# Performance work log

Hardware: AMD Instinct MI355X
Metric: run time of the kernel (lower is better)

The kernel has to match this reference:

```python
import jax, jax.numpy as jnp
import numpy as np
from jax import lax


def conv2d(x, w, b=None, pad=1):
    y = lax.conv_general_dilated(x, w, (1, 1), [(pad, pad), (pad, pad)],
                                 dimension_numbers=('NCHW', 'OIHW', 'NCHW'))
    return y if b is None else y + b[None, :, None, None]


def conv3d(x, w, b=None, pad=(0, 0, 0), dil=(1, 1, 1), groups=1):
    y = lax.conv_general_dilated(x, w, (1, 1, 1), [(p, p) for p in pad],
                                 rhs_dilation=dil,
                                 dimension_numbers=('NCDHW', 'OIDHW', 'NCDHW'),
                                 feature_group_count=groups)
    return y if b is None else y + b[None, :, None, None, None]


def base_grid(H, W, dtype):
    # normalized grid, channel 0 = x in [-1,1], channel 1 = y in [-1,1]
    gxn = 2.0 * jnp.arange(W, dtype=dtype) / max(W - 1, 1) - 1.0
    gyn = 2.0 * jnp.arange(H, dtype=dtype) / max(H - 1, 1) - 1.0
    return jnp.stack([jnp.broadcast_to(gxn[None, :], (H, W)),
                      jnp.broadcast_to(gyn[:, None], (H, W))], 0)


def grid_sample(img, grid):
    # img (N,C,H,W), grid (N,H,W,2) in [-1,1] (x,y); bilinear, zeros padding, align_corners=False
    N, C, H, W = img.shape
    gx = ((grid[..., 0] + 1.0) * W - 1.0) * 0.5
    gy = ((grid[..., 1] + 1.0) * H - 1.0) * 0.5
    x0 = jnp.floor(gx)
    y0 = jnp.floor(gy)
    wx = gx - x0
    wy = gy - y0

    def one(im, x0b, y0b, wxb, wyb):
        x0i = x0b.astype(jnp.int32)
        y0i = y0b.astype(jnp.int32)

        def samp(xi, yi):
            valid = (xi >= 0) & (xi < W) & (yi >= 0) & (yi < H)
            v = im[:, jnp.clip(yi, 0, H - 1), jnp.clip(xi, 0, W - 1)]
            return v * valid[None].astype(im.dtype)

        v00 = samp(x0i, y0i)
        v01 = samp(x0i + 1, y0i)
        v10 = samp(x0i, y0i + 1)
        v11 = samp(x0i + 1, y0i + 1)
        return (v00 * (1 - wxb) * (1 - wyb) + v01 * wxb * (1 - wyb)
                + v10 * (1 - wxb) * wyb + v11 * wxb * wyb)

    return jax.vmap(one)(img, x0, y0, wx, wy)


def ms_def_corr(x, y, off):
    # deformable correlation: per scale, warp y by that scale's offset and take
    # the channel-mean dot product with x -> (BT, S, H, W)
    BT, C, H, W = x.shape
    base = base_grid(H, W, x.dtype)
    sc = jnp.array([W - 1, H - 1], x.dtype)[None, :, None, None]
    S = off.shape[1] // 2
    corrs = []
    for i in range(S):
        vg = base[None] + off[:, 2 * i:2 * i + 2] / sc
        w = grid_sample(y, vg.transpose(0, 2, 3, 1))
        corrs.append(jnp.mean(x * w, axis=1))
    return jnp.stack(corrs, 1)


def corr_filter(corr, w1, w2):
    avg = jnp.mean(corr, 1, keepdims=True)
    mx = jnp.max(corr, 1, keepdims=True)
    var = jnp.var(corr, axis=1, keepdims=True, ddof=1)  # torch.var unbiased
    attn = jax.nn.sigmoid(conv2d(jnp.concatenate([avg, mx], 1), w1) + conv2d(var, w2))
    return corr * attn


def setup_inputs() -> dict:
    key = jax.random.key(0)
    ks = jax.random.split(key, 16)
    B, C, T, H, W = 2, 64, 16, 64, 64
    S = 3
    r = C // 16

    def n(k, shape, s=0.02):
        return jax.random.normal(k, shape, jnp.float32) * s

    return {
        'x': jax.random.normal(ks[0], (B, C, T, H, W), jnp.float32),
        'ofs_l_w1': n(ks[1], (C, 2 * C, 3, 3)), 'ofs_l_b1': jnp.zeros((C,), jnp.float32),
        'ofs_l_w2': n(ks[2], (2 * S, C, 3, 3)), 'ofs_l_b2': jnp.zeros((2 * S,), jnp.float32),
        'ofs_r_w1': n(ks[3], (C, 2 * C, 3, 3)), 'ofs_r_b1': jnp.zeros((C,), jnp.float32),
        'ofs_r_w2': n(ks[4], (2 * S, C, 3, 3)), 'ofs_r_b2': jnp.zeros((2 * S,), jnp.float32),
        'cf_w1': n(ks[5], (1, 2, 3, 3), 0.1), 'cf_w2': n(ks[6], (1, 1, 3, 3), 0.1),
        'down_w': n(ks[7], (r, C, 1, 1, 1), 0.1),
        'sa1_w': n(ks[8], (r, 1, 9, 3, 3), 0.1), 'sa1_b': jnp.zeros((r,), jnp.float32),
        'sa2_w': n(ks[9], (r, 1, 9, 3, 3), 0.1), 'sa2_b': jnp.zeros((r,), jnp.float32),
        'sa3_w': n(ks[10], (r, 1, 9, 3, 3), 0.1), 'sa3_b': jnp.zeros((r,), jnp.float32),
        'agg_w': jnp.ones((3,), jnp.float32) / 3,
        'back_w': n(ks[11], (C, r, 1, 1, 1), 0.1),
        'fusion_w': jnp.ones((2,), jnp.float32) / 2,
    }


def reference(x, ofs_l_w1, ofs_l_b1, ofs_l_w2, ofs_l_b2,
              ofs_r_w1, ofs_r_b1, ofs_r_w2, ofs_r_b2,
              cf_w1, cf_w2, down_w,
              sa1_w, sa1_b, sa2_w, sa2_b, sa3_w, sa3_b,
              agg_w, back_w, fusion_w):
    B, C, T, H, W = x.shape
    r = down_w.shape[0]

    # long-term branch: 1x1x1 down conv -> 3 dilated depthwise 3D convs -> 1x1x1 up conv
    x_agg = conv3d(x, down_w)
    agg = (conv3d(x_agg, sa1_w, sa1_b, (4, 1, 1), (1, 1, 1), r) * agg_w[0]
           + conv3d(x_agg, sa2_w, sa2_b, (4, 2, 2), (1, 2, 2), r) * agg_w[1]
           + conv3d(x_agg, sa3_w, sa3_b, (4, 3, 3), (1, 3, 3), r) * agg_w[2])
    long_term = jax.nn.sigmoid(conv3d(agg, back_w)) - 0.5

    # temporal shifts
    left = jnp.concatenate([x[:, :, 1:], x[:, :, -1:]], 2)
    right = jnp.concatenate([x[:, :, :1], x[:, :, :-1]], 2)
    xf = x.transpose(0, 2, 1, 3, 4).reshape(B * T, C, H, W)
    lf = left.transpose(0, 2, 1, 3, 4).reshape(B * T, C, H, W)
    rf = right.transpose(0, 2, 1, 3, 4).reshape(B * T, C, H, W)

    off_lm = conv2d(jax.nn.relu(conv2d(jnp.concatenate([xf, lf], 1), ofs_l_w1, ofs_l_b1)),
                    ofs_l_w2, ofs_l_b2)
    off_rm = conv2d(jax.nn.relu(conv2d(jnp.concatenate([xf, rf], 1), ofs_r_w1, ofs_r_b1)),
                    ofs_r_w2, ofs_r_b2)

    corr_lm = ms_def_corr(xf, lf, off_lm)
    corr_rm = ms_def_corr(xf, rf, off_rm)
    fcl = corr_filter(corr_lm, cf_w1, cf_w2)
    fcr = corr_filter(corr_rm, cf_w1, cf_w2)

    base = base_grid(H, W, x.dtype)
    sc = jnp.array([W - 1, H - 1], x.dtype)[None, :, None, None]
    vg_lm = base[None] + off_lm[:, :2] / sc
    vg_rm = base[None] + off_rm[:, :2] / sc
    warped_lm = grid_sample(lf, vg_lm.transpose(0, 2, 3, 1))
    warped_rm = grid_sample(rf, vg_rm.transpose(0, 2, 3, 1))

    attn_lm = jnp.mean(fcl, 1, keepdims=True)
    attn_rm = jnp.mean(fcr, 1, keepdims=True)
    feat_lm = warped_lm * (jax.nn.sigmoid(attn_lm) - 0.5)
    feat_rm = warped_rm * (jax.nn.sigmoid(attn_rm) - 0.5)

    short = fusion_w[0] * feat_lm + fusion_w[1] * feat_rm
    short = short.reshape(B, T, C, H, W).transpose(0, 2, 1, 3, 4)
    return short * long_term
```

## Files before the change

kernel.cpp:

```cpp
#include <hip/hip_runtime.h>
#include <hip/hip_bf16.h>
#include <math.h>


typedef __attribute__((ext_vector_type(8))) short short8v;
typedef __attribute__((ext_vector_type(4))) float f32x4;

__device__ __forceinline__ float sigmoidf_(float v) {
    return 1.0f / (1.0f + expf(-v));
}

__device__ __forceinline__ float bf2f(short s) {
    union { unsigned u; float f; } z;
    z.u = ((unsigned)(unsigned short)s) << 16;
    return z.f;
}

__device__ __forceinline__ void gll16(const __hip_bfloat16* g, __hip_bfloat16* l) {
    __builtin_amdgcn_global_load_lds((const __attribute__((address_space(1))) unsigned int*)(const void*)g,
                                     (__attribute__((address_space(3))) unsigned int*)(void*)l,
                                     16, 0, 0);
}

struct Samp { int o0, o1, o2, o3; float w0, w1, w2, w3; };

__device__ __forceinline__ Samp make_samp(float ox, float oy, int w, int h) {
    float bx = (2.0f * (float)w) / 63.0f - 1.0f;
    float by = (2.0f * (float)h) / 63.0f - 1.0f;
    float vx = bx + ox / 63.0f;
    float vy = by + oy / 63.0f;
    float gx = ((vx + 1.0f) * 64.0f - 1.0f) * 0.5f;
    float gy = ((vy + 1.0f) * 64.0f - 1.0f) * 0.5f;
    float fx = floorf(gx), fy = floorf(gy);
    float wx = gx - fx, wy = gy - fy;
    int x0 = (int)fx, y0 = (int)fy;
    int x1 = x0 + 1, y1 = y0 + 1;
    bool vx0 = (x0 >= 0) && (x0 < 64), vx1 = (x1 >= 0) && (x1 < 64);
    bool vy0 = (y0 >= 0) && (y0 < 64), vy1 = (y1 >= 0) && (y1 < 64);
    int cx0 = min(max(x0, 0), 63), cx1 = min(max(x1, 0), 63);
    int cy0 = min(max(y0, 0), 63), cy1 = min(max(y1, 0), 63);
    Samp s;
    s.o0 = cy0 * 4224 + (cx0 + 1) * 64; s.w0 = (1.0f - wx) * (1.0f - wy) * ((vx0 && vy0) ? 1.0f : 0.0f);
    s.o1 = cy0 * 4224 + (cx1 + 1) * 64; s.w1 = wx * (1.0f - wy) * ((vx1 && vy0) ? 1.0f : 0.0f);
    s.o2 = cy1 * 4224 + (cx0 + 1) * 64; s.w2 = (1.0f - wx) * wy * ((vx0 && vy1) ? 1.0f : 0.0f);
    s.o3 = cy1 * 4224 + (cx1 + 1) * 64; s.w3 = wx * wy * ((vx1 && vy1) ? 1.0f : 0.0f);
    return s;
}

__global__ __launch_bounds__(256) void k_prep_x(const float* __restrict__ x,
                                                const float* __restrict__ dw,
                                                __hip_bfloat16* __restrict__ xT,
                                                float* __restrict__ xa)
{
    int bid = blockIdx.x;
    int h = bid & 63;
    int n = bid >> 6;
    int b = n >> 4, t = n & 15;
    __shared__ float s[64][65];
    int tid = threadIdx.x;
    for (int idx = tid; idx < 4096; idx += 256) {
        int c = idx >> 6, w = idx & 63;
        s[c][w] = x[(((size_t)b * 64 + c) * 16 + t) * 4096 + h * 64 + w];
    }
    __syncthreads();
    __hip_bfloat16* op = xT + ((size_t)n * 64 + h) * 4224;
    for (int idx = tid; idx < 4224; idx += 256) {
        int wp = idx >> 6, c = idx & 63;
        float v = (wp == 0 || wp == 65) ? 0.f : s[c][wp - 1];
        op[idx] = __float2bfloat16(v);
    }
    int w = tid & 63, g = tid >> 6;
    float acc = 0.f;
    const float* dwg = dw + g * 64;
    #pragma unroll 8
    for (int c = 0; c < 64; c++) acc = fmaf(s[c][w], dwg[c], acc);
    xa[((size_t)(b * 4 + g) * 16 + t) * 4096 + h * 64 + w] = acc;
}

__global__ __launch_bounds__(256) void k_prep_w(const float* __restrict__ wl1,
                                                const float* __restrict__ wr1,
                                                const float* __restrict__ wl2,
                                                const float* __restrict__ wr2,
                                                __hip_bfloat16* __restrict__ Wmisc,
                                                __hip_bfloat16* __restrict__ hidden)
{
    int idx = blockIdx.x * 256 + threadIdx.x;
    if (idx < 147456) {
        int side = (idx >= 73728) ? 1 : 0;
        int i = idx - side * 73728;
        int ci = i & 127;
        int co = (i >> 7) & 63;
        int tap = i >> 13;
        const float* w = side ? wr1 : wl1;
        float v = w[((size_t)co * 128 + ci) * 9 + tap];
        int pos = side * 73728 + tap * 8192 + co * 128 + (ci ^ ((co & 15) << 3));
        Wmisc[pos] = __float2bfloat16(v);
    } else if (idx < 151680) {
        Wmisc[idx] = __float2bfloat16(0.f);
    } else if (idx < 170112) {
        int i2 = idx - 151680;
        int side = i2 / 9216;
        int j = i2 - side * 9216;
        int tap = j >> 10;
        int rem = j & 1023;
        int co = rem >> 6;
        int ci = rem & 63;
        const float* w = side ? wr2 : wl2;
        float v = (co < 6) ? w[((size_t)co * 64 + ci) * 9 + tap] : 0.f;
        Wmisc[idx] = __float2bfloat16(v);
    } else if (idx < 432256) {
        int i3 = idx - 170112;
        int co = i3 & 63;
        int sel = (i3 >> 6) & 1;
        int rr = (i3 >> 7) & 63;
        int nn = i3 >> 13;
        hidden[((size_t)(nn * 64 + rr) * 66 + (sel ? 65 : 0)) * 64 + co] = __float2bfloat16(0.f);
    }
}

__global__ __launch_bounds__(512, 4) void k_conv1_mfma(const __hip_bfloat16* __restrict__ xT,
                                                       const __hip_bfloat16* __restrict__ Wb,
                                                       const __hip_bfloat16* __restrict__ zrow,
                                                       const float* __restrict__ b1,
                                                       __hip_bfloat16* __restrict__ hidden,
                                                       int dir)
{
    __shared__ __hip_bfloat16 sB[24576];

    int bid = blockIdx.x;
    int rq = bid & 15;
    int n = bid >> 4;
    int b = n >> 4, t = n & 15;
    int t2 = (dir > 0) ? min(t + 1, 15) : max(t - 1, 0);
    int n2 = b * 16 + t2;

    int tid = threadIdx.x;
    int wv = tid >> 6;
    int lane = tid & 63;
    int r = rq * 4 + (wv & 3);
    int m0 = (wv >> 2) * 32;
    int lr = lane & 15;
    int q = lane >> 4;
    int lk = q << 3;

    const __hip_bfloat16* fA0 = xT + (size_t)n * 270336;
    const __hip_bfloat16* fA1 = xT + (size_t)n2 * 270336;

    f32x4 acc[2][4];
    #pragma unroll
    for (int ni = 0; ni < 4; ni++) {
        float bb = b1[ni * 16 + lr];
        acc[0][ni] = (f32x4){bb, bb, bb, bb};
        acc[1][ni] = (f32x4){bb, bb, bb, bb};
    }

    int kx[2][2];
    #pragma unroll
    for (int khalf = 0; khalf < 2; khalf++)
        #pragma unroll
        for (int ks = 0; ks < 2; ks++)
            kx[khalf][ks] = ((khalf << 7) + (ks << 6) + (q << 4)) ^ (lr << 4);

    const char* sbc = (const char*)&sB[0];

    #pragma unroll
    for (int g = 0; g < 3; g++) {
        __syncthreads();
        {
            const __hip_bfloat16* wsrc = Wb + (size_t)g * 24576 + wv * 3072 + lane * 8;
            #pragma unroll
            for (int j = 0; j < 6; j++)
                gll16(wsrc + j * 512, &sB[wv * 3072 + j * 512]);
        }
        __syncthreads();

        int rr = r + g - 1;
        bool ok = (rr >= 0) && (rr < 64);
        const __hip_bfloat16* r0 = ok ? (fA0 + rr * 4224) : zrow;
        const __hip_bfloat16* r1 = ok ? (fA1 + rr * 4224) : zrow;

        #pragma unroll
        for (int tl = 0; tl < 3; tl++) {
            int abase = (m0 + lr + tl) * 64 + lk;
            #pragma unroll
            for (int khalf = 0; khalf < 2; khalf++) {
                const __hip_bfloat16* ar = khalf ? r1 : r0;
                short8v a00 = *(const short8v*)(ar + abase);
                short8v a01 = *(const short8v*)(ar + abase + 32);
                short8v a10 = *(const short8v*)(ar + abase + 1024);
                short8v a11 = *(const short8v*)(ar + abase + 1056);
                #pragma unroll
                for (int ni = 0; ni < 4; ni++) {
                    int rowb = tl * 16384 + ni * 4096 + lr * 256;
                    short8v b0  = *(const short8v*)(sbc + (rowb + kx[khalf][0]));
                    short8v b1v = *(const short8v*)(sbc + (rowb + kx[khalf][1]));
                    acc[0][ni] = __builtin_amdgcn_mfma_f32_16x16x32_bf16(a00, b0, acc[0][ni], 0, 0, 0);
                    acc[1][ni] = __builtin_amdgcn_mfma_f32_16x16x32_bf16(a10, b0, acc[1][ni], 0, 0, 0);
                    acc[0][ni] = __builtin_amdgcn_mfma_f32_16x16x32_bf16(a01, b1v, acc[0][ni], 0, 0, 0);
                    acc[1][ni] = __builtin_amdgcn_mfma_f32_16x16x32_bf16(a11, b1v, acc[1][ni], 0, 0, 0);
                }
            }
        }
    }

    int pxq = q << 2;
    __hip_bfloat16* hb = hidden + (size_t)(n * 64 + r) * 66 * 64;
    #pragma unroll
    for (int mi = 0; mi < 2; mi++) {
        #pragma unroll
        for (int ni = 0; ni < 4; ni++) {
            int co = ni * 16 + lr;
            #pragma unroll
            for (int j = 0; j < 4; j++) {
                int px = m0 + mi * 16 + pxq + j;
                float v = acc[mi][ni][j];
                v = v < 0.f ? 0.f : v;
                hb[(size_t)(px + 1) * 64 + co] = __float2bfloat16(v);
            }
        }
    }
}

__global__ __launch_bounds__(256) void k_conv2_mfma(const __hip_bfloat16* __restrict__ hidden,
                                                    const __hip_bfloat16* __restrict__ W2b,
                                                    const __hip_bfloat16* __restrict__ zrow,
                                                    const float* __restrict__ b2,
                                                    float* __restrict__ off)
{
    int bid = blockIdx.x;
    int rq = bid & 15;
    int n = bid >> 4;
    int tid = threadIdx.x;
    int wv = tid >> 6;
    int lane = tid & 63;
    int r = rq * 4 + wv;
    int lr = lane & 15;
    int lk = (lane >> 4) << 3;

    const __hip_bfloat16* hbase = hidden + (size_t)n * 270336;

    float bb = (lr < 6) ? b2[lr] : 0.f;
    f32x4 acc[4];
    #pragma unroll
    for (int mi = 0; mi < 4; mi++) acc[mi] = (f32x4){bb, bb, bb, bb};

    #pragma unroll
    for (int tap = 0; tap < 9; tap++) {
        const int kh = tap / 3, kw = tap - (tap / 3) * 3;
        int rr = r + kh - 1;
        bool ok = (rr >= 0) && (rr < 64);
        const __hip_bfloat16* hr = ok ? (hbase + (size_t)rr * 4224) : zrow;
        const __hip_bfloat16* bw = W2b + ((size_t)tap * 16 + lr) * 64 + lk;
        short8v b0 = *(const short8v*)(bw);
        short8v b1v = *(const short8v*)(bw + 32);
        #pragma unroll
        for (int mi = 0; mi < 4; mi++) {
            int abase = (mi * 16 + lr + kw) * 64 + lk;
            short8v a0 = *(const short8v*)(hr + abase);
            short8v a1 = *(const short8v*)(hr + abase + 32);
            acc[mi] = __builtin_amdgcn_mfma_f32_16x16x32_bf16(a0, b0, acc[mi], 0, 0, 0);
            acc[mi] = __builtin_amdgcn_mfma_f32_16x16x32_bf16(a1, b1v, acc[mi], 0, 0, 0);
        }
    }
    if (lr < 6) {
        int pxq = (lane >> 4) << 2;
        #pragma unroll
        for (int mi = 0; mi < 4; mi++) {
            #pragma unroll
            for (int j = 0; j < 4; j++) {
                int px = mi * 16 + pxq + j;
                off[((size_t)n * 6 + lr) * 4096 + r * 64 + px] = acc[mi][j];
            }
        }
    }
}

__global__ __launch_bounds__(256) void k_agg(const float* __restrict__ xa,
                                             const float* __restrict__ w1, const float* __restrict__ b1,
                                             const float* __restrict__ w2, const float* __restrict__ b2,
                                             const float* __restrict__ w3, const float* __restrict__ b3,
                                             const float* __restrict__ aw,
                                             float* __restrict__ agg)
{
    int gid = blockIdx.x * 256 + threadIdx.x;
    int hw = gid & 4095;
    int rest = gid >> 12;
    int t = rest & 15;
    int g = (rest >> 4) & 3;
    int b = rest >> 6;
    int h = hw >> 6, w = hw & 63;
    const float* base = xa + ((size_t)(b * 4 + g) * 16) * 4096;
    const float* ws0 = w1 + g * 81;
    const float* ws1 = w2 + g * 81;
    const float* ws2 = w3 + g * 81;
    float acc0 = b1[g], acc1 = b2[g], acc2 = b3[g];
    for (int kd = 0; kd < 9; kd++) {
        int d = t + kd - 4;
        if (d < 0 || d > 15) continue;
        const float* fr = base + (size_t)d * 4096;
        #pragma unroll
        for (int kh = 0; kh < 3; kh++) {
            #pragma unroll
            for (int kw = 0; kw < 3; kw++) {
                int widx = kd * 9 + kh * 3 + kw;
                {
                    int yy = h + (kh - 1), xx = w + (kw - 1);
                    if (yy >= 0 && yy < 64 && xx >= 0 && xx < 64)
                        acc0 = fmaf(fr[yy * 64 + xx], ws0[widx], acc0);
                }
                {
                    int yy = h + (kh - 1) * 2, xx = w + (kw - 1) * 2;
                    if (yy >= 0 && yy < 64 && xx >= 0 && xx < 64)
                        acc1 = fmaf(fr[yy * 64 + xx], ws1[widx], acc1);
                }
                {
                    int yy = h + (kh - 1) * 3, xx = w + (kw - 1) * 3;
                    if (yy >= 0 && yy < 64 && xx >= 0 && xx < 64)
                        acc2 = fmaf(fr[yy * 64 + xx], ws2[widx], acc2);
                }
            }
        }
    }
    agg[gid] = acc0 * aw[0] + acc1 * aw[1] + acc2 * aw[2];
}

__global__ __launch_bounds__(256) void k_corr2(const __hip_bfloat16* __restrict__ xT,
                                               const float* __restrict__ off_l,
                                               const float* __restrict__ off_r,
                                               float* __restrict__ stats_l,
                                               float* __restrict__ stats_r)
{
    int gid0 = blockIdx.x * 256 + threadIdx.x;
    int half = gid0 >> 17;
    int gid = gid0 & 131071;
    const float* off = half ? off_r : off_l;
    float* stats = half ? stats_r : stats_l;

    int hw = gid & 4095;
    int n = gid >> 12;
    int b = n >> 4, t = n & 15;
    int t2 = half ? max(t - 1, 0) : min(t + 1, 15);
    int n2 = b * 16 + t2;
    int h = hw >> 6, w = hw & 63;

    const __hip_bfloat16* xf = xT + (size_t)n * 270336 + h * 4224 + (w + 1) * 64;
    const __hip_bfloat16* yf = xT + (size_t)n2 * 270336;

    Samp sp[3];
    #pragma unroll
    for (int s = 0; s < 3; s++) {
        float ox = off[((size_t)n * 6 + 2 * s) * 4096 + hw];
        float oy = off[((size_t)n * 6 + 2 * s + 1) * 4096 + hw];
        sp[s] = make_samp(ox, oy, w, h);
    }

    float ac[3][4];
    #pragma unroll
    for (int s = 0; s < 3; s++)
        #pragma unroll
        for (int qq = 0; qq < 4; qq++) ac[s][qq] = 0.f;

    for (int cc = 0; cc < 64; cc += 8) {
        short8v xv = *(const short8v*)(xf + cc);
        #pragma unroll
        for (int s = 0; s < 3; s++) {
            short8v v0 = *(const short8v*)(yf + sp[s].o0 + cc);
            short8v v1 = *(const short8v*)(yf + sp[s].o1 + cc);
            short8v v2 = *(const short8v*)(yf + sp[s].o2 + cc);
            short8v v3 = *(const short8v*)(yf + sp[s].o3 + cc);
            #pragma unroll
            for (int e = 0; e < 8; e++) {
                float xe = bf2f(xv[e]);
                ac[s][0] = fmaf(xe, bf2f(v0[e]), ac[s][0]);
                ac[s][1] = fmaf(xe, bf2f(v1[e]), ac[s][1]);
                ac[s][2] = fmaf(xe, bf2f(v2[e]), ac[s][2]);
                ac[s][3] = fmaf(xe, bf2f(v3[e]), ac[s][3]);
            }
        }
    }
    float c[3];
    #pragma unroll
    for (int s = 0; s < 3; s++)
        c[s] = (ac[s][0] * sp[s].w0 + ac[s][1] * sp[s].w1 + ac[s][2] * sp[s].w2 + ac[s][3] * sp[s].w3) * (1.0f / 64.0f);
    float avg = (c[0] + c[1] + c[2]) * (1.0f / 3.0f);
    float mx = fmaxf(c[0], fmaxf(c[1], c[2]));
    float d0 = c[0] - avg, d1 = c[1] - avg, d2 = c[2] - avg;
    float var = (d0 * d0 + d1 * d1 + d2 * d2) * 0.5f;
    stats[(size_t)n * 4096 + hw] = avg;
    stats[131072 + (size_t)n * 4096 + hw] = mx;
    stats[262144 + (size_t)n * 4096 + hw] = var;
}

__device__ __forceinline__ float attn_val(const float* __restrict__ stats, int n, int hw,
                                          const float* __restrict__ cfw1,
                                          const float* __restrict__ cfw2)
{
    int h = hw >> 6, w = hw & 63;
    const float* avg = stats + (size_t)n * 4096;
    const float* mx  = stats + 131072 + (size_t)n * 4096;
    const float* var = stats + 262144 + (size_t)n * 4096;
    float s = 0.f;
    #pragma unroll
    for (int k = 0; k < 9; k++) {
        int kh = k / 3 - 1, kw = k - (k / 3) * 3 - 1;
        int yy = h + kh, xx = w + kw;
        if (yy >= 0 && yy < 64 && xx >= 0 && xx < 64) {
            int p = yy * 64 + xx;
            s += avg[p] * cfw1[k] + mx[p] * cfw1[9 + k] + var[p] * cfw2[k];
        }
    }
    float attn = sigmoidf_(s);
    return sigmoidf_(avg[hw] * attn) - 0.5f;
}

__global__ __launch_bounds__(256) void k_final(const __hip_bfloat16* __restrict__ xT,
                                               const float* __restrict__ off_l,
                                               const float* __restrict__ off_r,
                                               const float* __restrict__ stats_l,
                                               const float* __restrict__ stats_r,
                                               const float* __restrict__ cfw1,
                                               const float* __restrict__ cfw2,
                                               const float* __restrict__ agg,
                                               const float* __restrict__ backw,
                                               const float* __restrict__ fusw,
                                               float* __restrict__ out)
{
    int gid = blockIdx.x * 256 + threadIdx.x;
    int hw = gid & 4095;
    int n = gid >> 12;
    int b = n >> 4, t = n & 15;
    int tl = min(t + 1, 15), tr = max(t - 1, 0);
    int nl = b * 16 + tl, nr = b * 16 + tr;
    int h = hw >> 6, w = hw & 63;

    float oxl = off_l[((size_t)n * 6 + 0) * 4096 + hw];
    float oyl = off_l[((size_t)n * 6 + 1) * 4096 + hw];
    float oxr = off_r[((size_t)n * 6 + 0) * 4096 + hw];
    float oyr = off_r[((size_t)n * 6 + 1) * 4096 + hw];
    Samp sl = make_samp(oxl, oyl, w, h);
    Samp sr = make_samp(oxr, oyr, w, h);

    const __hip_bfloat16* lf = xT + (size_t)nl * 270336;
    const __hip_bfloat16* rf = xT + (size_t)nr * 270336;

    float Al = attn_val(stats_l, n, hw, cfw1, cfw2) * fusw[0];
    float Ar = attn_val(stats_r, n, hw, cfw1, cfw2) * fusw[1];

    float ag0 = agg[((size_t)(b * 4 + 0) * 16 + t) * 4096 + hw];
    float ag1 = agg[((size_t)(b * 4 + 1) * 16 + t) * 4096 + hw];
    float ag2 = agg[((size_t)(b * 4 + 2) * 16 + t) * 4096 + hw];
    float ag3 = agg[((size_t)(b * 4 + 3) * 16 + t) * 4096 + hw];

    for (int cc = 0; cc < 64; cc += 8) {
        short8v l0 = *(const short8v*)(lf + sl.o0 + cc);
        short8v l1 = *(const short8v*)(lf + sl.o1 + cc);
        short8v l2 = *(const short8v*)(lf + sl.o2 + cc);
        short8v l3 = *(const short8v*)(lf + sl.o3 + cc);
        short8v r0 = *(const short8v*)(rf + sr.o0 + cc);
        short8v r1 = *(const short8v*)(rf + sr.o1 + cc);
        short8v r2 = *(const short8v*)(rf + sr.o2 + cc);
        short8v r3 = *(const short8v*)(rf + sr.o3 + cc);
        #pragma unroll
        for (int e = 0; e < 8; e++) {
            int c = cc + e;
            float wl = sl.w0 * bf2f(l0[e]) + sl.w1 * bf2f(l1[e]) + sl.w2 * bf2f(l2[e]) + sl.w3 * bf2f(l3[e]);
            float wr = sr.w0 * bf2f(r0[e]) + sr.w1 * bf2f(r1[e]) + sr.w2 * bf2f(r2[e]) + sr.w3 * bf2f(r3[e]);
            float lt = sigmoidf_(ag0 * backw[c * 4 + 0] + ag1 * backw[c * 4 + 1]
                               + ag2 * backw[c * 4 + 2] + ag3 * backw[c * 4 + 3]) - 0.5f;
            out[(((size_t)b * 64 + c) * 16 + t) * 4096 + hw] = (wl * Al + wr * Ar) * lt;
        }
    }
}

extern "C" void kernel_launch(void* const* d_in, const int* in_sizes, int n_in,
                              void* d_out, int out_size, void* d_ws, size_t ws_size,
                              hipStream_t stream)
{
    const float* x     = (const float*)d_in[0];
    const float* lw1   = (const float*)d_in[1];
    const float* lb1   = (const float*)d_in[2];
    const float* lw2   = (const float*)d_in[3];
    const float* lb2   = (const float*)d_in[4];
    const float* rw1   = (const float*)d_in[5];
    const float* rb1   = (const float*)d_in[6];
    const float* rw2   = (const float*)d_in[7];
    const float* rb2   = (const float*)d_in[8];
    const float* cfw1  = (const float*)d_in[9];
    const float* cfw2  = (const float*)d_in[10];
    const float* downw = (const float*)d_in[11];
    const float* sa1w  = (const float*)d_in[12];
    const float* sa1b  = (const float*)d_in[13];
    const float* sa2w  = (const float*)d_in[14];
    const float* sa2b  = (const float*)d_in[15];
    const float* sa3w  = (const float*)d_in[16];
    const float* sa3b  = (const float*)d_in[17];
    const float* aggw  = (const float*)d_in[18];
    const float* backw = (const float*)d_in[19];
    const float* fusw  = (const float*)d_in[20];
    float* out = (float*)d_out;

    float* ws      = (float*)d_ws;
    float* x_agg   = ws;
    float* agg     = x_agg + 524288;
    float* off_l   = agg + 524288;
    float* off_r   = off_l + 786432;
    float* stats_l = off_r + 786432;
    float* stats_r = stats_l + 393216;
    __hip_bfloat16* hidden = (__hip_bfloat16*)(stats_r + 393216);
    __hip_bfloat16* xT     = hidden + 8650752;
    __hip_bfloat16* Wmisc  = xT + 8650752;
    __hip_bfloat16* Wb     = Wmisc;
    __hip_bfloat16* zrow   = Wmisc + 147456;
    __hip_bfloat16* W2bL   = Wmisc + 151680;
    __hip_bfloat16* W2bR   = W2bL + 9216;

    k_prep_x<<<2048, 256, 0, stream>>>(x, downw, xT, x_agg);
    k_prep_w<<<1689, 256, 0, stream>>>(lw1, rw1, lw2, rw2, Wmisc, hidden);

    k_agg<<<2048, 256, 0, stream>>>(x_agg, sa1w, sa1b, sa2w, sa2b, sa3w, sa3b, aggw, agg);

    k_conv1_mfma<<<512, 512, 0, stream>>>(xT, Wb, zrow, lb1, hidden, +1);
    k_conv2_mfma<<<512, 256, 0, stream>>>(hidden, W2bL, zrow, lb2, off_l);

    k_conv1_mfma<<<512, 512, 0, stream>>>(xT, Wb + 73728, zrow, rb1, hidden, -1);
    k_conv2_mfma<<<512, 256, 0, stream>>>(hidden, W2bR, zrow, rb2, off_r);

    k_corr2<<<1024, 256, 0, stream>>>(xT, off_l, off_r, stats_l, stats_r);

    k_final<<<512, 256, 0, stream>>>(xT, off_l, off_r, stats_l, stats_r, cfw1, cfw2,
                                     agg, backw, fusw, out);
}
```

Before: 273.0 us.

## Split channel dimension across two threads in corr and final kernels

The correlation kernel now gives each pixel two lanes, each covering 32 of the 64 channels. It issues all gather loads up front and combines the partial dot products with a cross-lane shuffle. The final kernel likewise splits channels into two halves per pixel, preloading all bilinear taps before computing. Both launches double their grid. This raises memory-level parallelism and occupancy for these latency-bound gather kernels, at the cost of duplicated offset, attention and sample-setup work per pixel.

Result: faster. 258.5 us (-5.3%).

```diff
diff --git a/kernel.cpp b/kernel.cpp
--- a/kernel.cpp
+++ b/kernel.cpp
@@ -330,9 +330,14 @@
                                                float* __restrict__ stats_l,
                                                float* __restrict__ stats_r)
 {
-    int gid0 = blockIdx.x * 256 + threadIdx.x;
-    int half = gid0 >> 17;
-    int gid = gid0 & 131071;
+    int tid = threadIdx.x;
+    int wv = tid >> 6;
+    int lane = tid & 63;
+    int pl = lane & 31;
+    int ch = lane >> 5;
+    int pidx = blockIdx.x * 128 + wv * 32 + pl;
+    int half = pidx >> 17;
+    int gid = pidx & 131071;
     const float* off = half ? off_r : off_l;
     float* stats = half ? stats_r : stats_l;
 
@@ -342,9 +347,10 @@
     int t2 = half ? max(t - 1, 0) : min(t + 1, 15);
     int n2 = b * 16 + t2;
     int h = hw >> 6, w = hw & 63;
-
-    const __hip_bfloat16* xf = xT + (size_t)n * 270336 + h * 4224 + (w + 1) * 64;
-    const __hip_bfloat16* yf = xT + (size_t)n2 * 270336;
+    int cc0 = ch * 32;
+
+    const __hip_bfloat16* xf = xT + (size_t)n * 270336 + h * 4224 + (w + 1) * 64 + cc0;
+    const __hip_bfloat16* yf = xT + (size_t)n2 * 270336 + cc0;
 
     Samp sp[3];
     #pragma unroll
@@ -354,41 +360,59 @@
         sp[s] = make_samp(ox, oy, w, h);
     }
 
+    short8v xv[4];
+    #pragma unroll
+    for (int i = 0; i < 4; i++) xv[i] = *(const short8v*)(xf + 8 * i);
+
     float ac[3][4];
     #pragma unroll
     for (int s = 0; s < 3; s++)
         #pragma unroll
         for (int qq = 0; qq < 4; qq++) ac[s][qq] = 0.f;
 
-    for (int cc = 0; cc < 64; cc += 8) {
-        short8v xv = *(const short8v*)(xf + cc);
-        #pragma unroll
-        for (int s = 0; s < 3; s++) {
-            short8v v0 = *(const short8v*)(yf + sp[s].o0 + cc);
-            short8v v1 = *(const short8v*)(yf + sp[s].o1 + cc);
-            short8v v2 = *(const short8v*)(yf + sp[s].o2 + cc);
-            short8v v3 = *(const short8v*)(yf + sp[s].o3 + cc);
-            #pragma unroll
-            for (int e = 0; e < 8; e++) {
-                float xe = bf2f(xv[e]);
-                ac[s][0] = fmaf(xe, bf2f(v0[e]), ac[s][0]);
-                ac[s][1] = fmaf(xe, bf2f(v1[e]), ac[s][1]);
-                ac[s][2] = fmaf(xe, bf2f(v2[e]), ac[s][2]);
-                ac[s][3] = fmaf(xe, bf2f(v3[e]), ac[s][3]);
+    #pragma unroll
+    for (int s = 0; s < 3; s++) {
+        #pragma unroll
+        for (int pr = 0; pr < 2; pr++) {
+            int oa = pr ? sp[s].o2 : sp[s].o0;
+            int ob = pr ? sp[s].o3 : sp[s].o1;
+            short8v va[4], vb[4];
+            #pragma unroll
+            for (int i = 0; i < 4; i++) {
+                va[i] = *(const short8v*)(yf + oa + 8 * i);
+                vb[i] = *(const short8v*)(yf + ob + 8 * i);
             }
-        }
-    }
-    float c[3];
+            #pragma unroll
+            for (int i = 0; i < 4; i++) {
+                #pragma unroll
+                for (int e = 0; e < 8; e++) {
+                    float xe = bf2f(xv[i][e]);
+                    ac[s][pr * 2]     = fmaf(xe, bf2f(va[i][e]), ac[s][pr * 2]);
+                    ac[s][pr * 2 + 1] = fmaf(xe, bf2f(vb[i][e]), ac[s][pr * 2 + 1]);
+                }
+            }
+        }
+    }
+
     #pragma unroll
     for (int s = 0; s < 3; s++)
-        c[s] = (ac[s][0] * sp[s].w0 + ac[s][1] * sp[s].w1 + ac[s][2] * sp[s].w2 + ac[s][3] * sp[s].w3) * (1.0f / 64.0f);
-    float avg = (c[0] + c[1] + c[2]) * (1.0f / 3.0f);
-    float mx = fmaxf(c[0], fmaxf(c[1], c[2]));
-    float d0 = c[0] - avg, d1 = c[1] - avg, d2 = c[2] - avg;
-    float var = (d0 * d0 + d1 * d1 + d2 * d2) * 0.5f;
-    stats[(size_t)n * 4096 + hw] = avg;
-    stats[131072 + (size_t)n * 4096 + hw] = mx;
-    stats[262144 + (size_t)n * 4096 + hw] = var;
+        #pragma unroll
+        for (int qq = 0; qq < 4; qq++)
+            ac[s][qq] += __shfl_xor(ac[s][qq], 32, 64);
+
+    if (ch == 0) {
+        float c[3];
+        #pragma unroll
+        for (int s = 0; s < 3; s++)
+            c[s] = (ac[s][0] * sp[s].w0 + ac[s][1] * sp[s].w1 + ac[s][2] * sp[s].w2 + ac[s][3] * sp[s].w3) * (1.0f / 64.0f);
+        float avg = (c[0] + c[1] + c[2]) * (1.0f / 3.0f);
+        float mx = fmaxf(c[0], fmaxf(c[1], c[2]));
+        float d0 = c[0] - avg, d1 = c[1] - avg, d2 = c[2] - avg;
+        float var = (d0 * d0 + d1 * d1 + d2 * d2) * 0.5f;
+        stats[(size_t)n * 4096 + hw] = avg;
+        stats[131072 + (size_t)n * 4096 + hw] = mx;
+        stats[262144 + (size_t)n * 4096 + hw] = var;
+    }
 }
 
 __device__ __forceinline__ float attn_val(const float* __restrict__ stats, int n, int hw,
@@ -425,13 +449,15 @@
                                                const float* __restrict__ fusw,
                                                float* __restrict__ out)
 {
-    int gid = blockIdx.x * 256 + threadIdx.x;
-    int hw = gid & 4095;
-    int n = gid >> 12;
+    int gid0 = blockIdx.x * 256 + threadIdx.x;
+    int hw = gid0 & 4095;
+    int ch = (gid0 >> 12) & 1;
+    int n = gid0 >> 13;
     int b = n >> 4, t = n & 15;
     int tl = min(t + 1, 15), tr = max(t - 1, 0);
     int nl = b * 16 + tl, nr = b * 16 + tr;
     int h = hw >> 6, w = hw & 63;
+    int cc0 = ch * 32;
 
     float oxl = off_l[((size_t)n * 6 + 0) * 4096 + hw];
     float oyl = off_l[((size_t)n * 6 + 1) * 4096 + hw];
@@ -440,8 +466,21 @@
     Samp sl = make_samp(oxl, oyl, w, h);
     Samp sr = make_samp(oxr, oyr, w, h);
 
-    const __hip_bfloat16* lf = xT + (size_t)nl * 270336;
-    const __hip_bfloat16* rf = xT + (size_t)nr * 270336;
+    const __hip_bfloat16* lf = xT + (size_t)nl * 270336 + cc0;
+    const __hip_bfloat16* rf = xT + (size_t)nr * 270336 + cc0;
+
+    short8v lv[4][4], rv[4][4];
+    #pragma unroll
+    for (int i = 0; i < 4; i++) {
+        lv[0][i] = *(const short8v*)(lf + sl.o0 + 8 * i);
+        lv[1][i] = *(const short8v*)(lf + sl.o1 + 8 * i);
+        lv[2][i] = *(const short8v*)(lf + sl.o2 + 8 * i);
+        lv[3][i] = *(const short8v*)(lf + sl.o3 + 8 * i);
+        rv[0][i] = *(const short8v*)(rf + sr.o0 + 8 * i);
+        rv[1][i] = *(const short8v*)(rf + sr.o1 + 8 * i);
+        rv[2][i] = *(const short8v*)(rf + sr.o2 + 8 * i);
+        rv[3][i] = *(const short8v*)(rf + sr.o3 + 8 * i);
+    }
 
     float Al = attn_val(stats_l, n, hw, cfw1, cfw2) * fusw[0];
     float Ar = attn_val(stats_r, n, hw, cfw1, cfw2) * fusw[1];
@@ -451,20 +490,15 @@
     float ag2 = agg[((size_t)(b * 4 + 2) * 16 + t) * 4096 + hw];
     float ag3 = agg[((size_t)(b * 4 + 3) * 16 + t) * 4096 + hw];
 
-    for (int cc = 0; cc < 64; cc += 8) {
-        short8v l0 = *(const short8v*)(lf + sl.o0 + cc);
-        short8v l1 = *(const short8v*)(lf + sl.o1 + cc);
-        short8v l2 = *(const short8v*)(lf + sl.o2 + cc);
-        short8v l3 = *(const short8v*)(lf + sl.o3 + cc);
-        short8v r0 = *(const short8v*)(rf + sr.o0 + cc);
-        short8v r1 = *(const short8v*)(rf + sr.o1 + cc);
-        short8v r2 = *(const short8v*)(rf + sr.o2 + cc);
-        short8v r3 = *(const short8v*)(rf + sr.o3 + cc);
+    #pragma unroll
+    for (int i = 0; i < 4; i++) {
         #pragma unroll
         for (int e = 0; e < 8; e++) {
-            int c = cc + e;
-            float wl = sl.w0 * bf2f(l0[e]) + sl.w1 * bf2f(l1[e]) + sl.w2 * bf2f(l2[e]) + sl.w3 * bf2f(l3[e]);
-            float wr = sr.w0 * bf2f(r0[e]) + sr.w1 * bf2f(r1[e]) + sr.w2 * bf2f(r2[e]) + sr.w3 * bf2f(r3[e]);
+            int c = cc0 + i * 8 + e;
+            float wl = sl.w0 * bf2f(lv[0][i][e]) + sl.w1 * bf2f(lv[1][i][e])
+                     + sl.w2 * bf2f(lv[2][i][e]) + sl.w3 * bf2f(lv[3][i][e]);
+            float wr = sr.w0 * bf2f(rv[0][i][e]) + sr.w1 * bf2f(rv[1][i][e])
+                     + sr.w2 * bf2f(rv[2][i][e]) + sr.w3 * bf2f(rv[3][i][e]);
             float lt = sigmoidf_(ag0 * backw[c * 4 + 0] + ag1 * backw[c * 4 + 1]
                                + ag2 * backw[c * 4 + 2] + ag3 * backw[c * 4 + 3]) - 0.5f;
             out[(((size_t)b * 64 + c) * 16 + t) * 4096 + hw] = (wl * Al + wr * Ar) * lt;
@@ -525,8 +559,8 @@
     k_conv1_mfma<<<512, 512, 0, stream>>>(xT, Wb + 73728, zrow, rb1, hidden, -1);
     k_conv2_mfma<<<512, 256, 0, stream>>>(hidden, W2bR, zrow, rb2, off_r);
 
-    k_corr2<<<1024, 256, 0, stream>>>(xT, off_l, off_r, stats_l, stats_r);
-
-    k_final<<<512, 256, 0, stream>>>(xT, off_l, off_r, stats_l, stats_r, cfw1, cfw2,
-                                     agg, backw, fusw, out);
-}
+    k_corr2<<<2048, 256, 0, stream>>>(xT, off_l, off_r, stats_l, stats_r);
+
+    k_final<<<1024, 256, 0, stream>>>(xT, off_l, off_r, stats_l, stats_r, cfw1, cfw2,
+                                      agg, backw, fusw, out);
+}
```
